# Optimization experiments

Hardware: AMD Instinct MI355X
Metric: run time of the kernel (lower is better)

The kernel has to match this reference:

```python
import jax, jax.numpy as jnp
import numpy as np

EPS = 1e-5
GROUPS = 8


def conv2d(x, w, b, pad):
    y = jax.lax.conv_general_dilated(
        x, w, window_strides=(1, 1), padding=[(pad, pad), (pad, pad)],
        dimension_numbers=('NCHW', 'OIHW', 'NCHW'))
    return y + b[None, :, None, None]


def setup_inputs() -> dict:
    key = jax.random.key(0)
    ks = jax.random.split(key, 8)
    b, c, h, w = 32, 256, 56, 56
    cg = c // GROUPS
    x = jax.random.normal(ks[0], (b, c, h, w), dtype=jnp.float32)
    w1 = jax.random.normal(ks[1], (cg, cg, 1, 1), dtype=jnp.float32) * 0.05
    b1 = jnp.zeros((cg,), dtype=jnp.float32)
    w3a = jax.random.normal(ks[2], (cg, cg, 3, 3), dtype=jnp.float32) * 0.05
    b3a = jnp.zeros((cg,), dtype=jnp.float32)
    w3b = jax.random.normal(ks[3], (c, c, 3, 3), dtype=jnp.float32) * 0.02
    b3b = jnp.zeros((c,), dtype=jnp.float32)
    gn_w = jnp.ones((cg,), dtype=jnp.float32)
    gn_b = jnp.zeros((cg,), dtype=jnp.float32)
    return {"x": x, "w1": w1, "b1": b1, "w3a": w3a, "b3a": b3a,
            "w3b": w3b, "b3b": b3b, "gn_w": gn_w, "gn_b": gn_b}


def reference(x, w1, b1, w3a, b3a, w3b, b3b, gn_w, gn_b):
    b, c, h, w = x.shape
    cg = c // GROUPS
    bg = b * GROUPS
    gx = x.reshape(bg, cg, h, w)

    # spatial attention on grouped channels
    x_h = gx.mean(axis=3, keepdims=True)                       # [bg,cg,h,1]
    x_w = gx.mean(axis=2, keepdims=True).transpose(0, 1, 3, 2)  # [bg,cg,w,1]
    hw = conv2d(jnp.concatenate([x_h, x_w], axis=2), w1, b1, 0)
    xh, xw = hw[:, :, :h], hw[:, :, h:]
    x0 = gx * jax.nn.sigmoid(xh) * jax.nn.sigmoid(xw.transpose(0, 1, 3, 2))

    # GroupNorm with num_groups == num_channels (per-channel over HxW)
    mu = x0.mean(axis=(2, 3), keepdims=True)
    var = x0.var(axis=(2, 3), keepdims=True)
    x1 = (x0 - mu) / jnp.sqrt(var + EPS) * gn_w[None, :, None, None] + gn_b[None, :, None, None]

    x2 = conv2d(gx, w3a, b3a, 1)

    # channel softmax-matmul attention (per group)
    x11 = jax.nn.softmax(x1.mean(axis=(2, 3)), axis=-1)[:, None, :]  # [bg,1,cg]
    x12 = x1.reshape(bg, cg, h * w)
    x21 = jax.nn.softmax(x2.mean(axis=(2, 3)), axis=-1)[:, None, :]
    x22 = x2.reshape(bg, cg, h * w)
    weights1 = (jnp.matmul(x11, x22) + jnp.matmul(x21, x12)).reshape(bg, 1, h, w)

    # BatchNorm2d(affine=False), batch statistics (training mode)
    xr = x0.reshape(b, c, h, w)
    bm = xr.mean(axis=(0, 2, 3), keepdims=True)
    bv = xr.var(axis=(0, 2, 3), keepdims=True)
    x3 = (xr - bm) / jnp.sqrt(bv + EPS)

    x4 = conv2d(x, w3b, b3b, 1)

    # spatial softmax-matmul attention over full channels
    x31 = jax.nn.softmax(x3.mean(axis=1).reshape(b, 1, h * w), axis=-1)  # [b,1,hw]
    x32 = x3.reshape(b, c, h * w).transpose(0, 2, 1)                     # [b,hw,c]
    x41 = jax.nn.softmax(x4.mean(axis=1).reshape(b, 1, h * w), axis=-1)
    x42 = x4.reshape(b, c, h * w).transpose(0, 2, 1)
    weights2 = (jnp.matmul(x31, x42) + jnp.matmul(x41, x32)).reshape(b, c, 1, 1)

    return (gx * jax.nn.sigmoid(weights1)).reshape(b, c, h, w) + x * jax.nn.sigmoid(weights2)
```

## Files before the change

### kernel.cpp

```cpp
#include <hip/hip_runtime.h>
#include <math.h>

#define B  32
#define C  256
#define HH 56
#define WW 56
#define HW 3136
#define G  8
#define CG 32
#define BG 256
#define GC 8192
#define EPSF 1e-5f

typedef __attribute__((ext_vector_type(8))) short short8;
typedef __attribute__((ext_vector_type(4))) float f32x4;

#define GLOAD16(g, l) __builtin_amdgcn_global_load_lds( \
    (const __attribute__((address_space(1))) void*)(g), \
    (__attribute__((address_space(3))) void*)(l), 16, 0, 0)

__device__ __forceinline__ float sigmoidf_(float v){ return 1.0f/(1.0f+__expf(-v)); }
__device__ __forceinline__ unsigned short f2bf(float v){
  unsigned u = __builtin_bit_cast(unsigned, v);
  u = u + 0x7FFFu + ((u>>16)&1u);
  return (unsigned short)(u>>16);
}

__global__ void k1_rowcol(const float* __restrict__ x, float* __restrict__ rowm, float* __restrict__ colm){
  int gc = blockIdx.x;
  __shared__ float t[56][57];
  const float* xp = x + (size_t)gc*HW;
  for(int idx=threadIdx.x; idx<HW; idx+=blockDim.x) t[idx/56][idx%56] = xp[idx];
  __syncthreads();
  int tid = threadIdx.x;
  if(tid < 56){
    float s=0.f;
    #pragma unroll 8
    for(int j=0;j<56;j++) s+=t[tid][j];
    rowm[gc*56+tid] = s*(1.0f/56.0f);
  } else if(tid>=64 && tid<120){
    int j=tid-64; float s=0.f;
    #pragma unroll 8
    for(int i=0;i<56;i++) s+=t[i][j];
    colm[gc*56+j] = s*(1.0f/56.0f);
  }
}

__global__ void k2_hw(const float* __restrict__ rowm, const float* __restrict__ colm,
                      const float* __restrict__ w1, const float* __restrict__ b1,
                      float* __restrict__ sh, float* __restrict__ sw){
  int bg = blockIdx.x;
  __shared__ float inb[32][112];
  __shared__ float wt[32*32];
  __shared__ float bb[32];
  for(int idx=threadIdx.x; idx<32*56; idx+=blockDim.x){
    int ic=idx/56, p=idx%56;
    inb[ic][p]    = rowm[(bg*32+ic)*56+p];
    inb[ic][56+p] = colm[(bg*32+ic)*56+p];
  }
  for(int idx=threadIdx.x; idx<1024; idx+=blockDim.x) wt[idx]=w1[idx];
  if(threadIdx.x<32) bb[threadIdx.x]=b1[threadIdx.x];
  __syncthreads();
  for(int o=threadIdx.x; o<32*112; o+=blockDim.x){
    int oc=o/112, p=o%112;
    float s=bb[oc];
    #pragma unroll
    for(int ic=0;ic<32;ic++) s += wt[oc*32+ic]*inb[ic][p];
    float sg = sigmoidf_(s);
    if(p<56) sh[(bg*32+oc)*56+p]=sg; else sw[(bg*32+oc)*56+(p-56)]=sg;
  }
}

__global__ void k2b_x11(const float* __restrict__ gnb, const float* __restrict__ b3a, float* __restrict__ x11){
  __shared__ float v[32];
  if(threadIdx.x<32) v[threadIdx.x]=gnb[threadIdx.x];
  __syncthreads();
  if(threadIdx.x==0){
    float m=-1e30f; for(int i=0;i<32;i++) m=fmaxf(m,v[i]);
    float s=0.f; for(int i=0;i<32;i++){ v[i]=__expf(v[i]-m); s+=v[i]; }
    float d=0.f;
    for(int i=0;i<32;i++){ float p=v[i]/s; x11[i]=p; d+=p*b3a[i]; }
    x11[32]=d;
  }
}

__global__ void k3_stats(const float* __restrict__ x, const float* __restrict__ sh, const float* __restrict__ sw,
                         float* __restrict__ gsum, float* __restrict__ gsq){
  int gc=blockIdx.x;
  __shared__ float ssh[56], ssw[56];
  if(threadIdx.x<56) ssh[threadIdx.x]=sh[gc*56+threadIdx.x];
  else if(threadIdx.x>=64&&threadIdx.x<120) ssw[threadIdx.x-64]=sw[gc*56+threadIdx.x-64];
  __syncthreads();
  const float* xp=x+(size_t)gc*HW;
  float s=0.f,s2=0.f;
  for(int p=threadIdx.x;p<HW;p+=blockDim.x){
    float v=xp[p]*ssh[p/56]*ssw[p%56];
    s+=v; s2+=v*v;
  }
  for(int off=32;off>0;off>>=1){ s+=__shfl_down(s,off,64); s2+=__shfl_down(s2,off,64); }
  __shared__ float rs[4], rs2[4];
  int wid=threadIdx.x>>6, lane=threadIdx.x&63;
  if(lane==0){rs[wid]=s; rs2[wid]=s2;}
  __syncthreads();
  if(threadIdx.x==0){
    gsum[gc]=rs[0]+rs[1]+rs[2]+rs[3];
    gsq[gc]=rs2[0]+rs2[1]+rs2[2]+rs2[3];
  }
}

__global__ void k4a(const float* __restrict__ gsum, const float* __restrict__ gsq,
                    float* __restrict__ mu, float* __restrict__ istd){
  int gc=blockIdx.x*256+threadIdx.x;
  float m=gsum[gc]*(1.0f/HW);
  float v=gsq[gc]*(1.0f/HW)-m*m;
  mu[gc]=m; istd[gc]=rsqrtf(v+EPSF);
}

__global__ void k4b(const float* __restrict__ gsum, const float* __restrict__ gsq,
                    float* __restrict__ bm, float* __restrict__ binv){
  int c=threadIdx.x;
  float s=0.f,s2=0.f;
  for(int b=0;b<B;b++){ s+=gsum[b*256+c]; s2+=gsq[b*256+c]; }
  float m=s*(1.0f/(B*HW));
  float v=s2*(1.0f/(B*HW))-m*m;
  bm[c]=m; binv[c]=rsqrtf(v+EPSF);
}

__global__ __launch_bounds__(128) void k5m(const unsigned short* __restrict__ xt,
    const unsigned short* __restrict__ wta, const float* __restrict__ x11,
    float* __restrict__ w1a, float* __restrict__ cs2){
  __shared__ short Bs[6*58*32];
  int bid = blockIdx.x;
  int bg = bid / 14; int pt = bid % 14;
  int b = bg >> 3; int g = bg & 7;
  int i0 = pt*4;
  int tid = threadIdx.x;
  int lane = tid & 63, wv = tid >> 6;
  int q = lane >> 4, rl = lane & 15;
  const unsigned short* xb = xt + (size_t)b*58*58*256 + g*32;

  #pragma unroll
  for(int issue=0; issue<11; ++issue){
    int idx = issue*128 + tid;
    if(idx < 1392){
      int pl = idx >> 2, ch = idx & 3;
      int r = pl / 58, jj = pl - r*58;
      const unsigned short* src = xb + ((size_t)(i0 + r)*58 + jj)*256 + ch*8;
      GLOAD16(src, &Bs[idx*8]);
    }
  }
  __syncthreads();

  f32x4 acc[2][7];
  #pragma unroll
  for(int mi=0;mi<2;mi++)
    #pragma unroll
    for(int ni=0;ni<7;ni++) acc[mi][ni]=(f32x4){0.f,0.f,0.f,0.f};

  int pr[7], pj[7];
  #pragma unroll
  for(int ni=0;ni<7;ni++){
    int px = wv*112 + ni*16 + rl;
    pr[ni] = px/56; pj[ni] = px - pr[ni]*56;
  }

  for(int tap=0; tap<9; ++tap){
    int dy = tap/3, dx = tap - dy*3;
    short8 a[2], bfr[7];
    #pragma unroll
    for(int mi=0;mi<2;mi++)
      a[mi] = *(const short8*)(wta + tap*1024 + (mi*16+rl)*32 + q*8);
    #pragma unroll
    for(int ni=0;ni<7;ni++){
      int pix = (pr[ni] + dy)*58 + pj[ni] + dx;
      bfr[ni] = *(const short8*)&Bs[pix*32 + q*8];
    }
    #pragma unroll
    for(int mi=0;mi<2;mi++)
      #pragma unroll
      for(int ni=0;ni<7;ni++)
        acc[mi][ni] = __builtin_amdgcn_mfma_f32_16x16x32_bf16(a[mi], bfr[ni], acc[mi][ni], 0,0,0);
  }

  float x11v[2][4];
  #pragma unroll
  for(int mi=0;mi<2;mi++)
    #pragma unroll
    for(int r=0;r<4;r++) x11v[mi][r] = x11[mi*16 + q*4 + r];
  float x11b = x11[32];
  size_t pxg0 = (size_t)bg*HW + i0*56 + wv*112;
  #pragma unroll
  for(int ni=0;ni<7;ni++){
    float s=0.f;
    #pragma unroll
    for(int mi=0;mi<2;mi++)
      #pragma unroll
      for(int r=0;r<4;r++) s += x11v[mi][r]*acc[mi][ni][r];
    s += __shfl_xor(s,16,64);
    s += __shfl_xor(s,32,64);
    if(lane<16) w1a[pxg0 + ni*16 + lane] = s + x11b;
  }
  #pragma unroll
  for(int mi=0;mi<2;mi++){
    #pragma unroll
    for(int r=0;r<4;r++){
      float s=0.f;
      #pragma unroll
      for(int ni=0;ni<7;ni++) s += acc[mi][ni][r];
      s += __shfl_xor(s,1,64);
      s += __shfl_xor(s,2,64);
      s += __shfl_xor(s,4,64);
      s += __shfl_xor(s,8,64);
      if(rl==0) atomicAdd(&cs2[bg*32 + mi*16 + q*4 + r], s);
    }
  }
}

__global__ void k6(const float* __restrict__ cs2, const float* __restrict__ b3a,
                   const float* __restrict__ mu, const float* __restrict__ istd,
                   const float* __restrict__ gnw, const float* __restrict__ gnb,
                   float* __restrict__ av, float* __restrict__ cst){
  int bg=blockIdx.x; int t=threadIdx.x;
  float m = cs2[bg*32+t]*(1.0f/HW) + b3a[t];
  float mx=m;
  for(int off=16;off>0;off>>=1) mx=fmaxf(mx,__shfl_xor(mx,off,32));
  float e=__expf(m-mx);
  float s=e;
  for(int off=16;off>0;off>>=1) s+=__shfl_xor(s,off,32);
  float x21=e/s;
  int gc=bg*32+t;
  float is=istd[gc];
  av[gc]=x21*is*gnw[t];
  float cv=x21*(gnb[t]-mu[gc]*is*gnw[t]);
  for(int off=16;off>0;off>>=1) cv+=__shfl_xor(cv,off,32);
  if(t==0) cst[bg]=cv;
}

__global__ void k7(const float* __restrict__ x, const float* __restrict__ sh, const float* __restrict__ sw,
                   const float* __restrict__ w1a, const float* __restrict__ av, const float* __restrict__ cst,
                   const float* __restrict__ binv, float* __restrict__ weights1, float* __restrict__ s3pre){
  int b=blockIdx.x/56, i=blockIdx.x%56;
  int j=threadIdx.x;
  if(j>=56) return;
  float s3=0.f;
  for(int g=0;g<8;g++){
    int bg=b*8+g;
    float wsum=0.f;
    for(int cgi=0;cgi<32;cgi++){
      int gc=bg*32+cgi;
      int c=g*32+cgi;
      float x0=x[(size_t)gc*HW+i*56+j]*sh[gc*56+i]*sw[gc*56+j];
      wsum+=av[gc]*x0;
      s3+=binv[c]*x0;
    }
    weights1[(size_t)bg*HW+i*56+j]=w1a[(size_t)bg*HW+i*56+j]+wsum+cst[bg];
  }
  s3pre[(size_t)b*HW+i*56+j]=s3*(1.0f/256.0f);
}

__global__ void k_softmax_hw(const float* __restrict__ in, float* __restrict__ out, float scale){
  int b=blockIdx.x;
  const float* ip=in+(size_t)b*HW;
  float mx=-1e30f;
  for(int p=threadIdx.x;p<HW;p+=blockDim.x) mx=fmaxf(mx,ip[p]*scale);
  for(int off=32;off>0;off>>=1) mx=fmaxf(mx,__shfl_xor(mx,off,64));
  __shared__ float red[4];
  int wid=threadIdx.x>>6, lane=threadIdx.x&63;
  if(lane==0) red[wid]=mx;
  __syncthreads();
  mx=fmaxf(fmaxf(red[0],red[1]),fmaxf(red[2],red[3]));
  float s=0.f;
  for(int p=threadIdx.x;p<HW;p+=blockDim.x) s+=__expf(ip[p]*scale-mx);
  for(int off=32;off>0;off>>=1) s+=__shfl_down(s,off,64);
  __shared__ float red2[4];
  if(lane==0) red2[wid]=s;
  __syncthreads();
  s=red2[0]+red2[1]+red2[2]+red2[3];
  float inv=1.0f/s;
  for(int p=threadIdx.x;p<HW;p+=blockDim.x) out[(size_t)b*HW+p]=__expf(ip[p]*scale-mx)*inv;
}

__global__ void kxt(const float* __restrict__ x, unsigned short* __restrict__ xt){
  int bid = blockIdx.x;
  int b = bid / 196; int r2 = bid % 196; int icb = r2 / 49; int pxb = r2 % 49;
  __shared__ float t[64][65];
  int tid = threadIdx.x;
  #pragma unroll
  for(int k=0;k<16;k++){
    int e = k*256 + tid;
    int ic = e>>6, px = e&63;
    t[ic][px] = x[((size_t)(b*256 + icb*64 + ic))*HW + pxb*64 + px];
  }
  __syncthreads();
  #pragma unroll
  for(int k=0;k<16;k++){
    int e = k*256 + tid;
    int px = e>>6, ic = e&63;
    int pxg = pxb*64 + px;
    int pi = pxg/56, pj = pxg%56;
    xt[(((size_t)b*58 + pi + 1)*58 + pj + 1)*256 + icb*64 + ic] = f2bf(t[ic][px]);
  }
}

__global__ void kwt(const float* __restrict__ w3b, unsigned short* __restrict__ wt){
  int idx = blockIdx.x*256 + threadIdx.x;
  int tap = idx >> 16; int r = idx & 65535; int oc = r >> 8; int ic = r & 255;
  wt[idx] = f2bf(w3b[((size_t)oc*256 + ic)*9 + tap]);
}

__global__ void kwta(const float* __restrict__ w3a, unsigned short* __restrict__ wta){
  int idx = blockIdx.x*256 + threadIdx.x;
  if(idx < 9216){
    int tap = idx >> 10; int r = idx & 1023; int oc = r >> 5; int ic = r & 31;
    wta[idx] = f2bf(w3a[((size_t)oc*32 + ic)*9 + tap]);
  }
}

__global__ __launch_bounds__(512) void k9m(const unsigned short* __restrict__ xt,
    const unsigned short* __restrict__ wt, const float* __restrict__ x31,
    float* __restrict__ s4pre, float* __restrict__ w2a){
  __shared__ short Ab[2][128*32];
  __shared__ short Bb[2][224*32];
  int bid = blockIdx.x;
  int b = bid / 28; int rr = bid % 28; int pt = rr >> 1; int oct = rr & 1;
  int i0 = pt*4; int ocb = oct*128;
  int tid = threadIdx.x;
  int lane = tid & 63, wv = tid >> 6;
  int wm = wv & 3, wn = wv >> 2;
  int q = lane >> 4, rl = lane & 15;
  const unsigned short* xb = xt + (size_t)b*58*58*256;

  #define STAGE_A(BUF, TAP, IC0) do{ \
    int idx = tid; int oc_ = idx>>2, cs_ = idx&3; \
    const unsigned short* src = wt + (((size_t)(TAP)*256 + ocb + oc_)*256 + (IC0) + (((cs_ ^ ((oc_>>1)&3)))<<3)); \
    GLOAD16(src, &Ab[BUF][idx*8]); }while(0)
  #define STAGE_B(BUF, TAP, IC0) do{ \
    int dy_ = (TAP)/3, dx_ = (TAP)%3; \
    { int idx = tid; int px_ = idx>>2, cs_ = idx&3; int r_ = px_/56, j_ = px_ - r_*56; \
      const unsigned short* src = xb + ((size_t)((i0 + r_ + dy_)*58 + (j_ + dx_)))*256 + (IC0) + ((cs_ ^ ((px_>>1)&3))<<3); \
      GLOAD16(src, &Bb[BUF][idx*8]); } \
    if(tid < 384){ int idx = tid + 512; int px_ = idx>>2, cs_ = idx&3; int r_ = px_/56, j_ = px_ - r_*56; \
      const unsigned short* src = xb + ((size_t)((i0 + r_ + dy_)*58 + (j_ + dx_)))*256 + (IC0) + ((cs_ ^ ((px_>>1)&3))<<3); \
      GLOAD16(src, &Bb[BUF][idx*8]); } }while(0)

  STAGE_A(0, 0, 0);
  STAGE_B(0, 0, 0);
  __syncthreads();

  f32x4 acc[2][7];
  #pragma unroll
  for(int mi=0;mi<2;mi++)
    #pragma unroll
    for(int ni=0;ni<7;ni++) acc[mi][ni] = (f32x4){0.f,0.f,0.f,0.f};

  for(int t=0; t<72; ++t){
    int cur = t & 1;
    if(t+1 < 72){
      int tn = t+1; int tap = tn >> 3; int ic0 = (tn & 7) << 5;
      STAGE_A(cur^1, tap, ic0);
      STAGE_B(cur^1, tap, ic0);
    }
    short8 a[2], bf[7];
    #pragma unroll
    for(int mi=0;mi<2;mi++){
      int row = wm*32 + mi*16 + rl;
      int cs = q ^ ((row>>1)&3);
      a[mi] = *(const short8*)&Ab[cur][row*32 + cs*8];
    }
    #pragma unroll
    for(int ni=0;ni<7;ni++){
      int px = wn*112 + ni*16 + rl;
      int cs = q ^ ((px>>1)&3);
      bf[ni] = *(const short8*)&Bb[cur][px*32 + cs*8];
    }
    #pragma unroll
    for(int mi=0;mi<2;mi++)
      #pragma unroll
      for(int ni=0;ni<7;ni++)
        acc[mi][ni] = __builtin_amdgcn_mfma_f32_16x16x32_bf16(a[mi], bf[ni], acc[mi][ni], 0,0,0);
    __syncthreads();
  }
  #undef STAGE_A
  #undef STAGE_B

  size_t pxbase = (size_t)b*HW + i0*56 + wn*112;
  #pragma unroll
  for(int ni=0;ni<7;ni++){
    float s = 0.f;
    #pragma unroll
    for(int mi=0;mi<2;mi++){
      s += acc[mi][ni][0]+acc[mi][ni][1]+acc[mi][ni][2]+acc[mi][ni][3];
    }
    s += __shfl_xor(s, 16, 64);
    s += __shfl_xor(s, 32, 64);
    if(lane < 16) atomicAdd(&s4pre[pxbase + ni*16 + lane], s);
  }
  float x31v[7];
  #pragma unroll
  for(int ni=0;ni<7;ni++) x31v[ni] = x31[pxbase + ni*16 + rl];
  #pragma unroll
  for(int mi=0;mi<2;mi++){
    #pragma unroll
    for(int r=0;r<4;r++){
      float s = 0.f;
      #pragma unroll
      for(int ni=0;ni<7;ni++) s += x31v[ni]*acc[mi][ni][r];
      s += __shfl_xor(s, 1, 64);
      s += __shfl_xor(s, 2, 64);
      s += __shfl_xor(s, 4, 64);
      s += __shfl_xor(s, 8, 64);
      if(rl == 0) atomicAdd(&w2a[b*256 + ocb + wm*32 + mi*16 + q*4 + r], s);
    }
  }
}

__global__ void k11(const float* __restrict__ x, const float* __restrict__ sh, const float* __restrict__ sw,
                    const float* __restrict__ x41, const float* __restrict__ bm, const float* __restrict__ binv,
                    const float* __restrict__ w2a, const float* __restrict__ b3b, float* __restrict__ w2){
  int gc=blockIdx.x; int b=gc/256, c=gc%256;
  __shared__ float ssh[56], ssw[56];
  if(threadIdx.x<56) ssh[threadIdx.x]=sh[gc*56+threadIdx.x];
  else if(threadIdx.x>=64&&threadIdx.x<120) ssw[threadIdx.x-64]=sw[gc*56+threadIdx.x-64];
  __syncthreads();
  const float* xp=x+(size_t)gc*HW;
  const float* wp=x41+(size_t)b*HW;
  float s=0.f;
  for(int p=threadIdx.x;p<HW;p+=blockDim.x){
    float x0=xp[p]*ssh[p/56]*ssw[p%56];
    s+=wp[p]*x0;
  }
  for(int off=32;off>0;off>>=1) s+=__shfl_down(s,off,64);
  __shared__ float red[4];
  int wid=threadIdx.x>>6, lane=threadIdx.x&63;
  if(lane==0) red[wid]=s;
  __syncthreads();
  if(threadIdx.x==0){
    float t=red[0]+red[1]+red[2]+red[3];
    w2[gc]=w2a[gc]+b3b[c]+binv[c]*t-bm[c]*binv[c];
  }
}

__global__ void k12(const float* __restrict__ x, const float* __restrict__ weights1, const float* __restrict__ w2,
                    float* __restrict__ out){
  int gc=blockIdx.x; int bg=gc/32;
  float sg2=sigmoidf_(w2[gc]);
  const float* xp=x+(size_t)gc*HW;
  const float* w1p=weights1+(size_t)bg*HW;
  float* op=out+(size_t)gc*HW;
  for(int p=threadIdx.x;p<HW;p+=blockDim.x){
    float s1=sigmoidf_(w1p[p]);
    op[p]=xp[p]*(s1+sg2);
  }
}

extern "C" void kernel_launch(void* const* d_in, const int* in_sizes, int n_in,
                              void* d_out, int out_size, void* d_ws, size_t ws_size,
                              hipStream_t stream) {
  const float* x   = (const float*)d_in[0];
  const float* w1  = (const float*)d_in[1];
  const float* b1  = (const float*)d_in[2];
  const float* w3a = (const float*)d_in[3];
  const float* b3a = (const float*)d_in[4];
  const float* w3b = (const float*)d_in[5];
  const float* b3b = (const float*)d_in[6];
  const float* gnw = (const float*)d_in[7];
  const float* gnb = (const float*)d_in[8];
  float* out=(float*)d_out;
  float* ws=(float*)d_ws;

  float* rowm=ws;
  float* colm=rowm+458752;
  float* sh  =colm+458752;
  float* sw  =sh+458752;
  float* x11 =sw+458752;
  float* gsum=x11+64;
  float* gsq =gsum+8192;
  float* mu  =gsq+8192;
  float* istd=mu+8192;
  float* bm  =istd+8192;
  float* binv=bm+256;
  float* cs2 =binv+256;
  float* w1a =cs2+8192;
  float* av  =w1a+802816;
  float* cst =av+8192;
  float* s3  =cst+256;
  float* x31 =s3+100352;
  float* s4  =x31+100352;
  float* x41 =s4+100352;
  float* w2a =x41+100352;
  float* w2  =w2a+8192;
  float* wt1 =w2+8192;
  unsigned short* xt = (unsigned short*)(wt1 + 802816);
  unsigned short* wtb = xt + (size_t)32*58*58*256;
  unsigned short* wta = wtb + 589824;

  hipMemsetAsync(xt, 0, (size_t)32*58*58*256*2, stream);
  kxt<<<32*4*49,256,0,stream>>>(x, xt);
  kwt<<<2304,256,0,stream>>>(w3b, wtb);
  kwta<<<36,256,0,stream>>>(w3a, wta);

  k1_rowcol<<<GC,256,0,stream>>>(x,rowm,colm);
  k2_hw<<<BG,128,0,stream>>>(rowm,colm,w1,b1,sh,sw);
  k2b_x11<<<1,32,0,stream>>>(gnb,b3a,x11);
  k3_stats<<<GC,256,0,stream>>>(x,sh,sw,gsum,gsq);
  k4a<<<32,256,0,stream>>>(gsum,gsq,mu,istd);
  k4b<<<1,256,0,stream>>>(gsum,gsq,bm,binv);
  hipMemsetAsync(cs2,0,8192*sizeof(float),stream);
  k5m<<<256*14,128,0,stream>>>(xt,wta,x11,w1a,cs2);
  k6<<<BG,32,0,stream>>>(cs2,b3a,mu,istd,gnw,gnb,av,cst);
  k7<<<B*56,64,0,stream>>>(x,sh,sw,w1a,av,cst,binv,wt1,s3);
  k_softmax_hw<<<B,256,0,stream>>>(s3,x31,1.0f);
  hipMemsetAsync(w2a,0,8192*sizeof(float),stream);
  hipMemsetAsync(s4,0,(size_t)HW*B*sizeof(float),stream);
  k9m<<<32*28,512,0,stream>>>(xt,wtb,x31,s4,w2a);
  k_softmax_hw<<<B,256,0,stream>>>(s4,x41,1.0f/256.0f);
  k11<<<GC,256,0,stream>>>(x,sh,sw,x41,bm,binv,w2a,b3b,w2);
  k12<<<GC,256,0,stream>>>(x,wt1,w2,out);
}
```

Measured before the change: 425.6 us.

## Stage halo input tile once per channel chunk and stream weights from global

The 3x3 conv implicit-GEMM kernel now loads a 6x58 padded input halo tile per 32-channel chunk into LDS and reuses it across all nine taps, instead of restaging shifted pixel tiles for every tap. Weight fragments are read directly from global memory into registers with one-tap lookahead rather than being staged through LDS. This cuts global-to-LDS traffic and the number of barriers from 72 to 8 per block. The trade-off is exposed global-load latency on the A operand and possible LDS bank conflicts, since the XOR swizzle was dropped for the B reads.

```diff
diff --git a/kernel.cpp b/kernel.cpp
--- a/kernel.cpp
+++ b/kernel.cpp
@@ -319,8 +319,7 @@
 __global__ __launch_bounds__(512) void k9m(const unsigned short* __restrict__ xt,
     const unsigned short* __restrict__ wt, const float* __restrict__ x31,
     float* __restrict__ s4pre, float* __restrict__ w2a){
-  __shared__ short Ab[2][128*32];
-  __shared__ short Bb[2][224*32];
+  __shared__ short Bs[2][6*58*32];
   int bid = blockIdx.x;
   int b = bid / 28; int rr = bid % 28; int pt = rr >> 1; int oct = rr & 1;
   int i0 = pt*4; int ocb = oct*128;
@@ -330,21 +329,19 @@
   int q = lane >> 4, rl = lane & 15;
   const unsigned short* xb = xt + (size_t)b*58*58*256;
 
-  #define STAGE_A(BUF, TAP, IC0) do{ \
-    int idx = tid; int oc_ = idx>>2, cs_ = idx&3; \
-    const unsigned short* src = wt + (((size_t)(TAP)*256 + ocb + oc_)*256 + (IC0) + (((cs_ ^ ((oc_>>1)&3)))<<3)); \
-    GLOAD16(src, &Ab[BUF][idx*8]); }while(0)
-  #define STAGE_B(BUF, TAP, IC0) do{ \
-    int dy_ = (TAP)/3, dx_ = (TAP)%3; \
-    { int idx = tid; int px_ = idx>>2, cs_ = idx&3; int r_ = px_/56, j_ = px_ - r_*56; \
-      const unsigned short* src = xb + ((size_t)((i0 + r_ + dy_)*58 + (j_ + dx_)))*256 + (IC0) + ((cs_ ^ ((px_>>1)&3))<<3); \
-      GLOAD16(src, &Bb[BUF][idx*8]); } \
-    if(tid < 384){ int idx = tid + 512; int px_ = idx>>2, cs_ = idx&3; int r_ = px_/56, j_ = px_ - r_*56; \
-      const unsigned short* src = xb + ((size_t)((i0 + r_ + dy_)*58 + (j_ + dx_)))*256 + (IC0) + ((cs_ ^ ((px_>>1)&3))<<3); \
-      GLOAD16(src, &Bb[BUF][idx*8]); } }while(0)
-
-  STAGE_A(0, 0, 0);
-  STAGE_B(0, 0, 0);
+  #define STAGE(BUF, IC0) do{ \
+    _Pragma("unroll") \
+    for(int issue=0; issue<3; ++issue){ \
+      int idx = issue*512 + tid; \
+      if(idx < 1392){ \
+        int pl = idx >> 2, ch = idx & 3; \
+        int r_ = pl / 58, jj = pl - r_*58; \
+        const unsigned short* src = xb + ((size_t)(i0 + r_)*58 + jj)*256 + (IC0) + ch*8; \
+        GLOAD16(src, &Bs[BUF][idx*8]); \
+      } \
+    } }while(0)
+
+  STAGE(0, 0);
   __syncthreads();
 
   f32x4 acc[2][7];
@@ -353,35 +350,45 @@
     #pragma unroll
     for(int ni=0;ni<7;ni++) acc[mi][ni] = (f32x4){0.f,0.f,0.f,0.f};
 
-  for(int t=0; t<72; ++t){
-    int cur = t & 1;
-    if(t+1 < 72){
-      int tn = t+1; int tap = tn >> 3; int ic0 = (tn & 7) << 5;
-      STAGE_A(cur^1, tap, ic0);
-      STAGE_B(cur^1, tap, ic0);
-    }
-    short8 a[2], bf[7];
-    #pragma unroll
-    for(int mi=0;mi<2;mi++){
-      int row = wm*32 + mi*16 + rl;
-      int cs = q ^ ((row>>1)&3);
-      a[mi] = *(const short8*)&Ab[cur][row*32 + cs*8];
-    }
-    #pragma unroll
-    for(int ni=0;ni<7;ni++){
-      int px = wn*112 + ni*16 + rl;
-      int cs = q ^ ((px>>1)&3);
-      bf[ni] = *(const short8*)&Bb[cur][px*32 + cs*8];
-    }
-    #pragma unroll
-    for(int mi=0;mi<2;mi++)
+  int pr[7], pj[7];
+  #pragma unroll
+  for(int ni=0;ni<7;ni++){
+    int px = wn*112 + ni*16 + rl;
+    pr[ni] = px/56; pj[ni] = px - pr[ni]*56;
+  }
+  const unsigned short* arow0 = wt + ((size_t)(ocb + wm*32 + 0*16 + rl))*256 + q*8;
+  const unsigned short* arow1 = wt + ((size_t)(ocb + wm*32 + 1*16 + rl))*256 + q*8;
+
+  for(int ck=0; ck<8; ++ck){
+    int cur = ck & 1;
+    if(ck+1 < 8) STAGE(cur^1, (ck+1)*32);
+    int icoff = ck*32;
+    short8 a0 = *(const short8*)(arow0 + icoff);
+    short8 a1 = *(const short8*)(arow1 + icoff);
+    #pragma unroll
+    for(int tap=0; tap<9; ++tap){
+      int dy = tap/3, dx = tap - dy*3;
+      short8 na0, na1;
+      if(tap < 8){
+        na0 = *(const short8*)(arow0 + (size_t)(tap+1)*65536 + icoff);
+        na1 = *(const short8*)(arow1 + (size_t)(tap+1)*65536 + icoff);
+      }
+      short8 bfr[7];
       #pragma unroll
-      for(int ni=0;ni<7;ni++)
-        acc[mi][ni] = __builtin_amdgcn_mfma_f32_16x16x32_bf16(a[mi], bf[ni], acc[mi][ni], 0,0,0);
+      for(int ni=0;ni<7;ni++){
+        int pix = (pr[ni] + dy)*58 + pj[ni] + dx;
+        bfr[ni] = *(const short8*)&Bs[cur][pix*32 + q*8];
+      }
+      #pragma unroll
+      for(int ni=0;ni<7;ni++){
+        acc[0][ni] = __builtin_amdgcn_mfma_f32_16x16x32_bf16(a0, bfr[ni], acc[0][ni], 0,0,0);
+        acc[1][ni] = __builtin_amdgcn_mfma_f32_16x16x32_bf16(a1, bfr[ni], acc[1][ni], 0,0,0);
+      }
+      a0 = na0; a1 = na1;
+    }
     __syncthreads();
   }
-  #undef STAGE_A
-  #undef STAGE_B
+  #undef STAGE
 
   size_t pxbase = (size_t)b*HW + i0*56 + wn*112;
   #pragma unroll
```

After: 453.2 us. +6.5%, slower.
